# Kernel tuning notes

Hardware: AMD Instinct MI355X
Metric: run time of the kernel (lower is better)

## Reference

```python
import jax, jax.numpy as jnp
import numpy as np

EPS = 1e-6
N, CHANNEL, M, K, D = 4096, 1024, 8, 2048, 128


def setup_inputs() -> dict:
    key = jax.random.key(0)
    ks = jax.random.split(key, 7)
    std = float(np.sqrt(2.0 / (5.0 * CHANNEL / M)))  # matches nn.init.normal_ std in __init__
    return {
        "x": jax.random.normal(ks[0], (N, CHANNEL), dtype=jnp.float32),
        "codebook0": jax.random.normal(ks[1], (M, K, D), dtype=jnp.float32) * std,
        "codebook1": jax.random.normal(ks[2], (M, K, D), dtype=jnp.float32) * std,
        "temperature0": jnp.ones((M, 1), dtype=jnp.float32),
        "temperature1": jnp.ones((M, 1), dtype=jnp.float32),
        "u0": jax.random.uniform(ks[3], (N, M, K), dtype=jnp.float32),
        "u1": jax.random.uniform(ks[4], (N, M, K), dtype=jnp.float32),
    }


def _distance(z, codebook):
    # z: (n, m, d), codebook: (m, k, d) -> (n, m, k) squared euclidean
    x2 = jnp.sum(z * z, axis=-1, keepdims=True)          # (n, m, 1)
    c2 = jnp.sum(codebook * codebook, axis=-1)           # (m, k)
    inter = jnp.einsum('nmd,mkd->nmk', z, codebook)      # (n, m, k)
    return x2 + c2 - 2.0 * inter


def _level(x, codebook, temperature, u):
    # One _quantizerEncoder level with Identity heads.
    n = x.shape[0]
    m, k, d = codebook.shape
    z = x.reshape(n, m, d)
    scale = jnp.asarray(np.sqrt(k), dtype=x.dtype)
    # logit = -distance / sqrt(k) * LowerBound(temperature, Eps)
    logit = (-_distance(z, codebook) / scale) * jnp.maximum(temperature, EPS)
    # gumbel-softmax, tau=1.0, hard=True (permutationRate == 0 -> no permutation)
    uc = jnp.clip(u, EPS, 1.0 - EPS)
    gumbel = -jnp.log(-jnp.log(uc))
    y = jax.nn.softmax(logit + gumbel, axis=-1)          # (n, m, k)
    hard_idx = jnp.argmax(y, axis=-1)                    # (n, m)
    y_hard = jax.nn.one_hot(hard_idx, k, dtype=y.dtype)
    sample = y_hard + y - jax.lax.stop_gradient(y)       # straight-through
    # _multiCodebookDeQuantization.forward
    deq = jnp.einsum('nmk,mkd->nmd', sample, codebook).reshape(n, m * d)
    return sample, deq, logit


def reference(x, codebook0, codebook1, temperature0, temperature1, u0, u1):
    # Encoder pass (Identity latentStageEncoder/quantizationHead/latentHead)
    _, deq0, _ = _level(x, codebook0, temperature0, u0)
    x1 = x - deq0                                        # residual to next level
    _, deq1, _ = _level(x1, codebook1, temperature1, u1)
    # Decoder pass, reversed (Identity dequantizationHead/sideHead/restoreHead):
    # formerLevel = decode(level1); xHat = deq0 + sideHead(formerLevel)
    former = deq1
    xHat = deq0 + former
    return xHat
```

## Files before the change

kernel.cpp:

```cpp
#include <hip/hip_runtime.h>
#include <math.h>


namespace {
constexpr int Nn = 4096, Mm = 8, Kk = 2048, Dd = 128;
constexpr int MK = Mm * Kk;
constexpr double SQRTK = 45.254833995939045;
constexpr float MARGIN = 0.25f;

__device__ __forceinline__ double wsum_d(double v) {
#pragma unroll
  for (int o = 32; o > 0; o >>= 1) v += __shfl_xor(v, o);
  return v;
}
__device__ __forceinline__ float wsum_f(float v) {
#pragma unroll
  for (int o = 32; o > 0; o >>= 1) v += __shfl_xor(v, o);
  return v;
}
__device__ __forceinline__ float wmax_f(float v) {
#pragma unroll
  for (int o = 32; o > 0; o >>= 1) v = fmaxf(v, __shfl_xor(v, o));
  return v;
}

__device__ __forceinline__ float fast_gumbel(float u) {
  float uc = fminf(fmaxf(u, 1e-6f), (float)(1.0 - 1e-6));
  float a = __log2f(uc);
  float t = -0.69314718f * a;
  return -0.69314718f * __log2f(t);
}

__device__ __forceinline__ double gumbel_d(float u) {
  double uc = fmin(fmax((double)u, 1e-6), 1.0 - 1e-6);
  return -log(-log(uc));
}

__global__ __launch_bounds__(256) void c2_kernel(
    const float* __restrict__ cb0, const float* __restrict__ cb1,
    double* __restrict__ c2d0, double* __restrict__ c2d1,
    float* __restrict__ c2f0, float* __restrict__ c2f1,
    float* __restrict__ sf0, float* __restrict__ sf1) {
  int wid = threadIdx.x >> 6, lane = threadIdx.x & 63;
  int row = blockIdx.x * 4 + wid;
  const float* cb = (row < MK) ? cb0 : cb1;
  int r = row & (MK - 1);
  float2 c = ((const float2*)(cb + (size_t)r * Dd))[lane];
  double s = (double)c.x * (double)c.x + (double)c.y * (double)c.y;
  s = wsum_d(s);
  if (lane == 0) {
    if (row < MK) { c2d0[r] = s; c2f0[r] = (float)s; sf0[r] = (float)sqrt(s); }
    else          { c2d1[r] = s; c2f1[r] = (float)s; sf1[r] = (float)sqrt(s); }
  }
}

template <bool L1>
__global__ __launch_bounds__(256) void level_kernel(
    const float* __restrict__ x,
    const float* __restrict__ cb,
    const float* __restrict__ cb_prev,
    const int* __restrict__ idx_prev,
    const float* __restrict__ temp,
    const float* __restrict__ u,
    const double* __restrict__ c2d,
    const float* __restrict__ c2f,
    const float* __restrict__ sf,
    int* __restrict__ idx_out,
    float* __restrict__ out)
{
  const int wid = threadIdx.x >> 6, lane = threadIdx.x & 63;
  const int p = blockIdx.x * 4 + wid;
  const int m = p >> 12;
  const int n = p & 4095;

  float2 z = ((const float2*)(x + (size_t)n * 1024 + m * Dd))[lane];
  float2 dq0 = make_float2(0.f, 0.f);
  if (L1) {
    int i0 = idx_prev[p];
    dq0 = ((const float2*)(cb_prev + ((size_t)m * Kk + i0) * Dd))[lane];
    z.x -= dq0.x; z.y -= dq0.y;
  }
  float zn = sqrtf(wsum_f(z.x * z.x + z.y * z.y));
  double wd = (double)fmaxf(temp[m], 1e-6f) / SQRTK;
  float wf = (float)wd;
  float tzn = 2.0f * zn;

  const float* urow = u + ((size_t)n * Mm + m) * Kk;
  const float4* u4 = (const float4*)urow;
  const float4* c24 = (const float4*)(c2f + m * Kk);
  const float4* s4 = (const float4*)(sf + m * Kk);

  float ub[32];
  float lbmax = -1e30f;
#pragma unroll
  for (int j = 0; j < 8; ++j) {
    float4 uu = u4[j * 64 + lane];
    float4 cc = c24[j * 64 + lane];
    float4 ss = s4[j * 64 + lane];
    float g0 = fast_gumbel(uu.x), g1 = fast_gumbel(uu.y);
    float g2 = fast_gumbel(uu.z), g3 = fast_gumbel(uu.w);
    float p0 = tzn * ss.x, p1 = tzn * ss.y, p2 = tzn * ss.z, p3 = tzn * ss.w;
    ub[j * 4 + 0] = g0 - (cc.x - p0) * wf;  lbmax = fmaxf(lbmax, g0 - (cc.x + p0) * wf);
    ub[j * 4 + 1] = g1 - (cc.y - p1) * wf;  lbmax = fmaxf(lbmax, g1 - (cc.y + p1) * wf);
    ub[j * 4 + 2] = g2 - (cc.z - p2) * wf;  lbmax = fmaxf(lbmax, g2 - (cc.z + p2) * wf);
    ub[j * 4 + 3] = g3 - (cc.w - p3) * wf;  lbmax = fmaxf(lbmax, g3 - (cc.w + p3) * wf);
  }
  float thr = wmax_f(lbmax) - MARGIN;

  double bestS = -1e300;
  int bestK = 0;
  const double* c2row = c2d + m * Kk;
  const float* cbm = cb + (size_t)m * Kk * Dd;
#pragma unroll
  for (int j = 0; j < 8; ++j) {
#pragma unroll
    for (int q = 0; q < 4; ++q) {
      unsigned long long mask = __ballot(ub[j * 4 + q] >= thr);
      while (mask) {
        int l = (int)__ffsll(mask) - 1;
        mask &= mask - 1;
        int kc = j * 256 + l * 4 + q;
        float2 c = ((const float2*)(cbm + (size_t)kc * Dd))[lane];
        double dot = wsum_d((double)z.x * (double)c.x + (double)z.y * (double)c.y);
        double sc = (2.0 * dot - c2row[kc]) * wd + gumbel_d(urow[kc]);
        if (sc > bestS) { bestS = sc; bestK = kc; }
      }
    }
  }

  if (L1) {
    float2 c1 = ((const float2*)(cbm + (size_t)bestK * Dd))[lane];
    ((float2*)(out + (size_t)n * 1024 + m * Dd))[lane] =
        make_float2(dq0.x + c1.x, dq0.y + c1.y);
  } else {
    if (lane == 0) idx_out[p] = bestK;
  }
}
}

extern "C" void kernel_launch(void* const* d_in, const int* in_sizes, int n_in,
                              void* d_out, int out_size, void* d_ws, size_t ws_size,
                              hipStream_t stream) {
  const float* x   = (const float*)d_in[0];
  const float* cb0 = (const float*)d_in[1];
  const float* cb1 = (const float*)d_in[2];
  const float* t0  = (const float*)d_in[3];
  const float* t1  = (const float*)d_in[4];
  const float* u0  = (const float*)d_in[5];
  const float* u1  = (const float*)d_in[6];
  float* out = (float*)d_out;

  char* ws = (char*)d_ws;
  double* c2d0 = (double*)ws;
  double* c2d1 = c2d0 + MK;
  float* c2f0 = (float*)(c2d1 + MK);
  float* c2f1 = c2f0 + MK;
  float* sf0 = c2f1 + MK;
  float* sf1 = sf0 + MK;
  int* idx0 = (int*)(sf1 + MK);

  c2_kernel<<<8192, 256, 0, stream>>>(cb0, cb1, c2d0, c2d1, c2f0, c2f1, sf0, sf1);
  level_kernel<false><<<8192, 256, 0, stream>>>(x, cb0, nullptr, nullptr, t0, u0,
                                                c2d0, c2f0, sf0, idx0, nullptr);
  level_kernel<true><<<8192, 256, 0, stream>>>(x, cb1, cb0, idx0, t1, u1,
                                               c2d1, c2f1, sf1, nullptr, out);
}
```

Baseline: 635.8 us.

## Fuse both quantizer levels into one kernel with packed precomputed bounds

Merges the two per-level kernels into one fused kernel, so the level-0 index no longer goes through global memory and one launch is dropped. The prep kernel now folds the temperature scale into packed float2 (c2*w, 2*sqrt(c2)*w) bounds, which cuts per-candidate arithmetic and the separate array loads. Candidate refinement moves from a fixed 32 ballot passes to a single loop that takes one candidate at a time from a per-lane bitmask. The fused kernel keeps both levels' work in one thread's lifetime and adds a launch-bounds occupancy hint, which may raise register pressure.

New measurement: 623.3 us. Within noise of the previous version (-2.0%).

```diff
diff --git a/kernel.cpp b/kernel.cpp
--- a/kernel.cpp
+++ b/kernel.cpp
@@ -25,116 +25,122 @@
 }
 
 __device__ __forceinline__ float fast_gumbel(float u) {
-  float uc = fminf(fmaxf(u, 1e-6f), (float)(1.0 - 1e-6));
-  float a = __log2f(uc);
-  float t = -0.69314718f * a;
+  float uc = fminf(fmaxf(u, 1e-6f), 0.999999f);
+  float t = -0.69314718f * __log2f(uc);
   return -0.69314718f * __log2f(t);
 }
-
 __device__ __forceinline__ double gumbel_d(float u) {
   double uc = fmin(fmax((double)u, 1e-6), 1.0 - 1e-6);
   return -log(-log(uc));
 }
 
-__global__ __launch_bounds__(256) void c2_kernel(
+__global__ __launch_bounds__(256) void prep_kernel(
     const float* __restrict__ cb0, const float* __restrict__ cb1,
-    double* __restrict__ c2d0, double* __restrict__ c2d1,
-    float* __restrict__ c2f0, float* __restrict__ c2f1,
-    float* __restrict__ sf0, float* __restrict__ sf1) {
+    const float* __restrict__ t0, const float* __restrict__ t1,
+    float2* __restrict__ AS0, float2* __restrict__ AS1,
+    double* __restrict__ c2d0, double* __restrict__ c2d1) {
   int wid = threadIdx.x >> 6, lane = threadIdx.x & 63;
   int row = blockIdx.x * 4 + wid;
-  const float* cb = (row < MK) ? cb0 : cb1;
+  int lvl = row >= MK;
   int r = row & (MK - 1);
+  int m = r >> 11;
+  const float* cb = lvl ? cb1 : cb0;
+  const float* tp = lvl ? t1 : t0;
   float2 c = ((const float2*)(cb + (size_t)r * Dd))[lane];
   double s = (double)c.x * (double)c.x + (double)c.y * (double)c.y;
   s = wsum_d(s);
   if (lane == 0) {
-    if (row < MK) { c2d0[r] = s; c2f0[r] = (float)s; sf0[r] = (float)sqrt(s); }
-    else          { c2d1[r] = s; c2f1[r] = (float)s; sf1[r] = (float)sqrt(s); }
+    float wf = (float)((double)fmaxf(tp[m], 1e-6f) / SQRTK);
+    float2 as;
+    as.x = (float)s * wf;
+    as.y = 2.0f * (float)sqrt(s) * wf;
+    if (lvl) { c2d1[r] = s; AS1[r] = as; }
+    else     { c2d0[r] = s; AS0[r] = as; }
   }
 }
 
-template <bool L1>
-__global__ __launch_bounds__(256) void level_kernel(
+__device__ __forceinline__ int argmax_level(
+    float zx, float zy, int lane,
+    const float* __restrict__ cbm,
+    const float* __restrict__ urow,
+    const float2* __restrict__ ASm,
+    const double* __restrict__ c2m,
+    double wd) {
+  float zn = sqrtf(wsum_f(zx * zx + zy * zy));
+  const float4* u4 = (const float4*)urow;
+  const float4* as4 = (const float4*)ASm;
+
+  float ub[32];
+  float lbmax = -1e30f;
+#pragma unroll
+  for (int j = 0; j < 8; ++j) {
+    float4 uu = u4[j * 64 + lane];
+    float4 a0 = as4[(j * 64 + lane) * 2];
+    float4 a1 = as4[(j * 64 + lane) * 2 + 1];
+    float g0 = fast_gumbel(uu.x), g1 = fast_gumbel(uu.y);
+    float g2 = fast_gumbel(uu.z), g3 = fast_gumbel(uu.w);
+    float s0 = zn * a0.y, s1 = zn * a0.w, s2 = zn * a1.y, s3 = zn * a1.w;
+    float b0 = g0 - a0.x, b1 = g1 - a0.z, b2 = g2 - a1.x, b3 = g3 - a1.z;
+    ub[j * 4 + 0] = b0 + s0; lbmax = fmaxf(lbmax, b0 - s0);
+    ub[j * 4 + 1] = b1 + s1; lbmax = fmaxf(lbmax, b1 - s1);
+    ub[j * 4 + 2] = b2 + s2; lbmax = fmaxf(lbmax, b2 - s2);
+    ub[j * 4 + 3] = b3 + s3; lbmax = fmaxf(lbmax, b3 - s3);
+  }
+  float thr = wmax_f(lbmax) - MARGIN;
+
+  unsigned mask32 = 0;
+#pragma unroll
+  for (int t = 0; t < 32; ++t) mask32 |= (ub[t] >= thr ? 1u : 0u) << t;
+
+  double bestS = -1e300;
+  int bestK = 0;
+  while (true) {
+    unsigned long long wm = __ballot(mask32 != 0);
+    if (!wm) break;
+    int l = (int)__ffsll(wm) - 1;
+    unsigned lm = (unsigned)__shfl((int)mask32, l);
+    int t = __builtin_ffs((int)lm) - 1;
+    if (lane == l) mask32 &= mask32 - 1;
+    int kc = ((t >> 2) << 8) + (l << 2) + (t & 3);
+    float2 c = ((const float2*)(cbm + (size_t)kc * Dd))[lane];
+    double dot = wsum_d((double)zx * (double)c.x + (double)zy * (double)c.y);
+    double sc = (2.0 * dot - c2m[kc]) * wd + gumbel_d(urow[kc]);
+    if (sc > bestS) { bestS = sc; bestK = kc; }
+  }
+  return bestK;
+}
+
+__global__ __launch_bounds__(256, 4) void fused_kernel(
     const float* __restrict__ x,
-    const float* __restrict__ cb,
-    const float* __restrict__ cb_prev,
-    const int* __restrict__ idx_prev,
-    const float* __restrict__ temp,
-    const float* __restrict__ u,
-    const double* __restrict__ c2d,
-    const float* __restrict__ c2f,
-    const float* __restrict__ sf,
-    int* __restrict__ idx_out,
-    float* __restrict__ out)
-{
+    const float* __restrict__ cb0, const float* __restrict__ cb1,
+    const float* __restrict__ t0, const float* __restrict__ t1,
+    const float* __restrict__ u0, const float* __restrict__ u1,
+    const float2* __restrict__ AS0, const float2* __restrict__ AS1,
+    const double* __restrict__ c2d0, const double* __restrict__ c2d1,
+    float* __restrict__ out) {
   const int wid = threadIdx.x >> 6, lane = threadIdx.x & 63;
   const int p = blockIdx.x * 4 + wid;
   const int m = p >> 12;
   const int n = p & 4095;
 
   float2 z = ((const float2*)(x + (size_t)n * 1024 + m * Dd))[lane];
-  float2 dq0 = make_float2(0.f, 0.f);
-  if (L1) {
-    int i0 = idx_prev[p];
-    dq0 = ((const float2*)(cb_prev + ((size_t)m * Kk + i0) * Dd))[lane];
-    z.x -= dq0.x; z.y -= dq0.y;
-  }
-  float zn = sqrtf(wsum_f(z.x * z.x + z.y * z.y));
-  double wd = (double)fmaxf(temp[m], 1e-6f) / SQRTK;
-  float wf = (float)wd;
-  float tzn = 2.0f * zn;
+  double wd0 = (double)fmaxf(t0[m], 1e-6f) / SQRTK;
+  double wd1 = (double)fmaxf(t1[m], 1e-6f) / SQRTK;
 
-  const float* urow = u + ((size_t)n * Mm + m) * Kk;
-  const float4* u4 = (const float4*)urow;
-  const float4* c24 = (const float4*)(c2f + m * Kk);
-  const float4* s4 = (const float4*)(sf + m * Kk);
+  const float* u0row = u0 + ((size_t)n * Mm + m) * Kk;
+  const float* u1row = u1 + ((size_t)n * Mm + m) * Kk;
+  const float* cb0m = cb0 + (size_t)m * Kk * Dd;
+  const float* cb1m = cb1 + (size_t)m * Kk * Dd;
 
-  float ub[32];
-  float lbmax = -1e30f;
-#pragma unroll
-  for (int j = 0; j < 8; ++j) {
-    float4 uu = u4[j * 64 + lane];
-    float4 cc = c24[j * 64 + lane];
-    float4 ss = s4[j * 64 + lane];
-    float g0 = fast_gumbel(uu.x), g1 = fast_gumbel(uu.y);
-    float g2 = fast_gumbel(uu.z), g3 = fast_gumbel(uu.w);
-    float p0 = tzn * ss.x, p1 = tzn * ss.y, p2 = tzn * ss.z, p3 = tzn * ss.w;
-    ub[j * 4 + 0] = g0 - (cc.x - p0) * wf;  lbmax = fmaxf(lbmax, g0 - (cc.x + p0) * wf);
-    ub[j * 4 + 1] = g1 - (cc.y - p1) * wf;  lbmax = fmaxf(lbmax, g1 - (cc.y + p1) * wf);
-    ub[j * 4 + 2] = g2 - (cc.z - p2) * wf;  lbmax = fmaxf(lbmax, g2 - (cc.z + p2) * wf);
-    ub[j * 4 + 3] = g3 - (cc.w - p3) * wf;  lbmax = fmaxf(lbmax, g3 - (cc.w + p3) * wf);
-  }
-  float thr = wmax_f(lbmax) - MARGIN;
+  int b0 = argmax_level(z.x, z.y, lane, cb0m, u0row, AS0 + m * Kk, c2d0 + m * Kk, wd0);
+  float2 c0 = ((const float2*)(cb0m + (size_t)b0 * Dd))[lane];
 
-  double bestS = -1e300;
-  int bestK = 0;
-  const double* c2row = c2d + m * Kk;
-  const float* cbm = cb + (size_t)m * Kk * Dd;
-#pragma unroll
-  for (int j = 0; j < 8; ++j) {
-#pragma unroll
-    for (int q = 0; q < 4; ++q) {
-      unsigned long long mask = __ballot(ub[j * 4 + q] >= thr);
-      while (mask) {
-        int l = (int)__ffsll(mask) - 1;
-        mask &= mask - 1;
-        int kc = j * 256 + l * 4 + q;
-        float2 c = ((const float2*)(cbm + (size_t)kc * Dd))[lane];
-        double dot = wsum_d((double)z.x * (double)c.x + (double)z.y * (double)c.y);
-        double sc = (2.0 * dot - c2row[kc]) * wd + gumbel_d(urow[kc]);
-        if (sc > bestS) { bestS = sc; bestK = kc; }
-      }
-    }
-  }
+  float zx1 = z.x - c0.x, zy1 = z.y - c0.y;
+  int b1 = argmax_level(zx1, zy1, lane, cb1m, u1row, AS1 + m * Kk, c2d1 + m * Kk, wd1);
+  float2 c1 = ((const float2*)(cb1m + (size_t)b1 * Dd))[lane];
 
-  if (L1) {
-    float2 c1 = ((const float2*)(cbm + (size_t)bestK * Dd))[lane];
-    ((float2*)(out + (size_t)n * 1024 + m * Dd))[lane] =
-        make_float2(dq0.x + c1.x, dq0.y + c1.y);
-  } else {
-    if (lane == 0) idx_out[p] = bestK;
-  }
+  ((float2*)(out + (size_t)n * 1024 + m * Dd))[lane] =
+      make_float2(c0.x + c1.x, c0.y + c1.y);
 }
 }
 
@@ -151,17 +157,12 @@
   float* out = (float*)d_out;
 
   char* ws = (char*)d_ws;
-  double* c2d0 = (double*)ws;
+  float2* AS0 = (float2*)ws;
+  float2* AS1 = AS0 + MK;
+  double* c2d0 = (double*)(AS1 + MK);
   double* c2d1 = c2d0 + MK;
-  float* c2f0 = (float*)(c2d1 + MK);
-  float* c2f1 = c2f0 + MK;
-  float* sf0 = c2f1 + MK;
-  float* sf1 = sf0 + MK;
-  int* idx0 = (int*)(sf1 + MK);
 
-  c2_kernel<<<8192, 256, 0, stream>>>(cb0, cb1, c2d0, c2d1, c2f0, c2f1, sf0, sf1);
-  level_kernel<false><<<8192, 256, 0, stream>>>(x, cb0, nullptr, nullptr, t0, u0,
-                                                c2d0, c2f0, sf0, idx0, nullptr);
-  level_kernel<true><<<8192, 256, 0, stream>>>(x, cb1, cb0, idx0, t1, u1,
-                                               c2d1, c2f1, sf1, nullptr, out);
+  prep_kernel<<<8192, 256, 0, stream>>>(cb0, cb1, t0, t1, AS0, AS1, c2d0, c2d1);
+  fused_kernel<<<8192, 256, 0, stream>>>(x, cb0, cb1, t0, t1, u0, u1,
+                                         AS0, AS1, c2d0, c2d1, out);
 }
```
